# Optimization experiments

Measured on AMD Instinct MI355X. Metric: run time of the kernel, lower is better.

## Reference

```python
import jax, jax.numpy as jnp
import numpy as np

N = 100000        # nodes (== node_num)
E = 3200000       # edges
C = 8             # hidden (sparse=False branch)
HEADS = 2
GROUPS = 8
LAYERS = 3
FEAT = 16
EMB = 8
NCLS = 2


def glin(x, W, b):
    # PyG grouped Linear: x [..., C], W [G, C//G, C//G], b [C]
    G, cin, cout = W.shape
    xg = x.reshape(*x.shape[:-1], G, cin)
    out = jnp.einsum('...gi,gio->...go', xg, W)
    return out.reshape(*x.shape[:-1], G * cout) + b


def gcn_norm(edge_index, num_nodes):
    # symmetric GCN normalization with added self-loops, unit edge weights
    loop = jnp.arange(num_nodes, dtype=edge_index.dtype)
    src = jnp.concatenate([edge_index[0], loop])
    dst = jnp.concatenate([edge_index[1], loop])
    w = jnp.ones(src.shape[0], dtype=jnp.float32)
    deg = jax.ops.segment_sum(w, dst, num_segments=num_nodes)
    dinv = jnp.where(deg > 0, jax.lax.rsqrt(deg), 0.0)
    return src, dst, dinv[src] * dinv[dst]


def dna_conv(x_all, src, dst, norm, Wq, bq, Wk, bk, Wv, bv):
    # PyG DNAConv (eval mode): target's latest history entry attends over the
    # source neighbor's full history. x_all: [N, L, C].
    n, L, c = x_all.shape
    d = c // HEADS
    # q/k/v linears are per-entry -> compute per node, gather per edge (same math)
    q = glin(x_all[:, -1], Wq, bq).reshape(n, HEADS, d)    # [N,H,d]
    k = glin(x_all, Wk, bk).reshape(n, L, HEADS, d)        # [N,L,H,d]
    v = glin(x_all, Wv, bv).reshape(n, L, HEADS, d)
    qe = q[dst]                                            # [E',H,d]
    score = jnp.einsum('ehd,elhd->ehl', qe, k[src]) * (1.0 / np.sqrt(d))
    attn = jax.nn.softmax(score, axis=-1)                  # softmax over history L
    out = jnp.einsum('ehl,elhd->ehd', attn, v[src]).reshape(-1, c)
    out = out * norm[:, None]
    return jax.ops.segment_sum(out, dst, num_segments=n)   # aggr='add' at target


def setup_inputs():
    ks = jax.random.split(jax.random.key(0), 16)
    s = 0.5
    return {
        'x': jax.random.normal(ks[0], (N, FEAT), dtype=jnp.float32),
        'node_index': jnp.arange(N),
        'node_one_hot': jnp.zeros((N,), dtype=jnp.int32),
        'edge_index': jax.random.randint(ks[1], (2, E), 0, N),
        'edge_weight': jax.random.uniform(ks[2], (E,), dtype=jnp.float32),
        'emb_table': jax.random.normal(ks[3], (N, EMB), dtype=jnp.float32) * 0.1,
        'W1': jax.random.normal(ks[4], (EMB + FEAT, C), dtype=jnp.float32) * 0.2,
        'b1': jnp.zeros((C,), dtype=jnp.float32),
        'Wq': jax.random.normal(ks[5], (LAYERS, GROUPS, C // GROUPS, C // GROUPS), dtype=jnp.float32) * s,
        'bq': jnp.zeros((LAYERS, C), dtype=jnp.float32),
        'Wk': jax.random.normal(ks[6], (LAYERS, GROUPS, C // GROUPS, C // GROUPS), dtype=jnp.float32) * s,
        'bk': jnp.zeros((LAYERS, C), dtype=jnp.float32),
        'Wv': jax.random.normal(ks[7], (LAYERS, GROUPS, C // GROUPS, C // GROUPS), dtype=jnp.float32) * s,
        'bv': jnp.zeros((LAYERS, C), dtype=jnp.float32),
        'W2': jax.random.normal(ks[8], (C, NCLS), dtype=jnp.float32) * 0.3,
        'b2': jnp.zeros((NCLS,), dtype=jnp.float32),
    }


def reference(x, node_index, node_one_hot, edge_index, edge_weight,
              emb_table, W1, b1, Wq, bq, Wk, bk, Wv, bv, W2, b2):
    # node_one_hot / edge_weight are unpacked but unused in the original forward
    h = jnp.concatenate([emb_table[node_index], x], axis=1)   # [N, EMB+FEAT]
    h = jax.nn.relu(h @ W1 + b1)                              # [N, C]
    x_all = h[:, None, :]                                     # history [N, 1, C]
    src, dst, norm = gcn_norm(edge_index, x.shape[0])
    for i in range(LAYERS):
        h = jax.nn.relu(dna_conv(x_all, src, dst, norm,
                                 Wq[i], bq[i], Wk[i], bk[i], Wv[i], bv[i]))
        x_all = jnp.concatenate([x_all, h[:, None, :]], axis=1)
    logits = x_all[:, -1] @ W2 + b2
    return jax.nn.log_softmax(logits, axis=-1)
```

## Files before the change

### kernel.cpp

```cpp
#include <hip/hip_runtime.h>
#include <math.h>


#define SBB   8
#define SBN   256
#define CH    4096
#define CAP   9216

typedef _Float16 half8 __attribute__((ext_vector_type(8)));
typedef int int4v __attribute__((ext_vector_type(4)));

__global__ void __launch_bounds__(256) phaseAC(const int* __restrict__ eidx,
                                               int* __restrict__ gcnt,
                                               int* __restrict__ ebuf,
                                               int E, int NS) {
    __shared__ int sorted_[CH];
    __shared__ unsigned short karr[CH];
    __shared__ int cntS[512];
    __shared__ int lofs[512];
    __shared__ int wbase[512];
    __shared__ int sA[512], sB[512];
    int t = threadIdx.x, b = blockIdx.x;
    int base = b * CH;
    int nEdge = E - base; if (nEdge > CH) nEdge = CH;

    for (int i = t; i < 512; i += 256) cntS[i] = 0;
    __syncthreads();

    int w[16]; short kk[16];
#pragma unroll
    for (int it = 0; it < 4; it++) {
        int e0 = base + (it * 256 + t) * 4;
        if (e0 + 3 < E) {
            int4v s4 = __builtin_nontemporal_load((const int4v*)(eidx + e0));
            int4v d4 = __builtin_nontemporal_load((const int4v*)(eidx + E + e0));
#pragma unroll
            for (int j = 0; j < 4; j++) {
                int idx = it * 4 + j;
                w[idx] = s4[j] | ((d4[j] & (SBN - 1)) << 17);
                kk[idx] = (short)(d4[j] >> SBB);
                atomicAdd(&cntS[kk[idx]], 1);
            }
        } else {
#pragma unroll
            for (int j = 0; j < 4; j++) {
                int e = e0 + j, idx = it * 4 + j;
                if (e < E) {
                    int s = eidx[e], d = eidx[E + e];
                    w[idx] = s | ((d & (SBN - 1)) << 17);
                    kk[idx] = (short)(d >> SBB);
                    atomicAdd(&cntS[kk[idx]], 1);
                } else { w[idx] = 0; kk[idx] = 511; }
            }
        }
    }
    __syncthreads();
    sA[t] = cntS[t]; sA[t + 256] = cntS[t + 256];
    __syncthreads();
    int* sp = sA; int* dp = sB;
    for (int o = 1; o < 512; o <<= 1) {
#pragma unroll
        for (int h = 0; h < 2; h++) {
            int i = t + h * 256;
            int v = sp[i];
            if (i >= o) v += sp[i - o];
            dp[i] = v;
        }
        __syncthreads();
        int* tmp = sp; sp = dp; dp = tmp;
    }
    for (int i = t; i < 512; i += 256) {
        int excl = sp[i] - cntS[i];
        lofs[i] = excl;
        if (i < NS && cntS[i] > 0) {
            int g = atomicAdd(&gcnt[i], cntS[i]);
            wbase[i] = i * CAP + g - excl;
        }
    }
    __syncthreads();
#pragma unroll
    for (int idx = 0; idx < 16; idx++) {
        if (kk[idx] != 511) {
            int p = atomicAdd(&lofs[kk[idx]], 1);
            sorted_[p] = w[idx];
            karr[p] = (unsigned short)kk[idx];
        }
    }
    __syncthreads();
    for (int i = t; i < nEdge; i += 256)
        ebuf[wbase[karr[i]] + i] = sorted_[i];
}

__global__ void super_csr(int* __restrict__ ebuf, const int* __restrict__ gcnt,
                          unsigned int* __restrict__ off, char* __restrict__ A,
                          char* __restrict__ U, int NS, int n) {
    __shared__ int seg[CAP];
    __shared__ int cnt[SBN];
    __shared__ int fillp[SBN];
    __shared__ int sd[256];
    int t = threadIdx.x, k = blockIdx.x;
    cnt[t] = 0;
    int start = k * CAP;
    int len = gcnt[k];
    __syncthreads();
    for (int i = t; i < len; i += 256) {
        int w = __builtin_nontemporal_load(&ebuf[start + i]);
        seg[i] = w;
        atomicAdd(&cnt[w >> 17], 1);
    }
    __syncthreads();
    int v = cnt[t];
    sd[t] = v; __syncthreads();
    for (int o = 1; o < 256; o <<= 1) {
        int u = 0; if (t >= o) u = sd[t - o];
        __syncthreads(); sd[t] += u; __syncthreads();
    }
    int excl = sd[t] - v;
    fillp[t] = excl;
    int d = (k << SBB) + t;
    if (d < n) {
        off[d] = (unsigned int)(start + excl) | ((unsigned int)v << 22);
        float dvv = rsqrtf((float)(v + 1));
        *(float*)(A + (size_t)d * 32 + 16) = dvv;
        *(float*)(U + (size_t)d * 64 + 48) = dvv;
    }
    __syncthreads();
    for (int i = t; i < len; i += 256) {
        int w = seg[i];
        int pos = atomicAdd(&fillp[w >> 17], 1);
        ebuf[start + pos] = w & 131071;
    }
}

__global__ void node_init(const float* __restrict__ x, const int* __restrict__ nidx,
                          const float* __restrict__ emb, const float* __restrict__ W1,
                          const float* __restrict__ b1, char* __restrict__ A,
                          char* __restrict__ U, int* __restrict__ gcnt,
                          int NS, int n) {
    int i = blockIdx.x * blockDim.x + threadIdx.x;
    if (i < NS) gcnt[i] = 0;
    if (i >= n) return;
    float in[24];
    int ni = nidx[i];
    const float4* ep = (const float4*)(emb + (size_t)ni * 8);
    float4 e0 = ep[0], e1 = ep[1];
    in[0] = e0.x; in[1] = e0.y; in[2] = e0.z; in[3] = e0.w;
    in[4] = e1.x; in[5] = e1.y; in[6] = e1.z; in[7] = e1.w;
    const float4* xp = (const float4*)(x + (size_t)i * 16);
#pragma unroll
    for (int t = 0; t < 4; t++) {
        float4 v = xp[t];
        in[8 + 4 * t + 0] = v.x; in[8 + 4 * t + 1] = v.y;
        in[8 + 4 * t + 2] = v.z; in[8 + 4 * t + 3] = v.w;
    }
    float acc[8];
#pragma unroll
    for (int j = 0; j < 8; j++) acc[j] = b1[j];
#pragma unroll
    for (int t = 0; t < 24; t++) {
        float xv = in[t];
#pragma unroll
        for (int j = 0; j < 8; j++) acc[j] = fmaf(xv, W1[t * 8 + j], acc[j]);
    }
    half8 h;
#pragma unroll
    for (int j = 0; j < 8; j++) h[j] = (_Float16)fmaxf(acc[j], 0.0f);
    *(half8*)(A + (size_t)i * 32) = h;
    *(half8*)(U + (size_t)i * 64) = h;
}

template <int Li, bool LAST>
__global__ void __launch_bounds__(256, 2)
agg_layer(const int* __restrict__ ssrc, const unsigned int* __restrict__ off,
          const char* __restrict__ A, char* __restrict__ U,
          const float* __restrict__ wq, const float* __restrict__ bq,
          const float* __restrict__ wk, const float* __restrict__ bk,
          const float* __restrict__ wv, const float* __restrict__ bv,
          const float* __restrict__ W2, const float* __restrict__ b2,
          float* __restrict__ out, int n) {
    constexpr int B = 8;
    int tid = blockIdx.x * blockDim.x + threadIdx.x;
    int d = tid >> 3, t = tid & 7;
    if (d >= n) return;
    unsigned int ow = off[d];
    int lo = (int)(ow & 0x3FFFFFu), cnt = (int)(ow >> 22);

    float qk[8];
    if (Li >= 2) {
        half8 qh = (Li == 2) ? *(const half8*)(U + (size_t)d * 64 + 16)
                             : *(const half8*)(U + (size_t)d * 64 + 32);
#pragma unroll
        for (int c = 0; c < 8; c++) {
            float qv = fmaf((float)qh[c], wq[c], bq[c]);
            qk[c] = 0.5f * wk[c] * qv;
        }
    }

    float T[8]; float SN = 0.f;
#pragma unroll
    for (int c = 0; c < 8; c++) T[c] = 0.f;

    int total = cnt + 1;
    int g = (total + 7) >> 3;
    int j0 = t * g;
    int j1 = j0 + g; if (j1 > total) j1 = total;

    for (int j = j0; j < j1; j += B) {
        int m = j1 - j; if (m > B) m = B;
        int sidx[B];
#pragma unroll
        for (int u = 0; u < B; u++) {
            int idx = j + u;
            sidx[u] = (u < m) ? ((idx == 0) ? d : ssrc[lo + idx - 1]) : d;
        }
        half8 r[B][Li]; float nsv[B];
#pragma unroll
        for (int u = 0; u < B; u++) {
            if (u < m) {
                if (Li == 1) {
                    const char* p = A + (size_t)sidx[u] * 32;
                    r[u][0] = *(const half8*)p;
                    nsv[u] = *(const float*)(p + 16);
                } else {
                    const char* p = U + (size_t)sidx[u] * 64;
#pragma unroll
                    for (int l = 0; l < Li; l++) r[u][l] = *(const half8*)(p + l * 16);
                    nsv[u] = *(const float*)(p + 48);
                }
            }
        }
#pragma unroll
        for (int u = 0; u < B; u++) {
            if (u < m) {
                float xs[8 * Li];
#pragma unroll
                for (int l = 0; l < Li; l++)
#pragma unroll
                    for (int c = 0; c < 8; c++) xs[l * 8 + c] = (float)r[u][l][c];
                float ns = nsv[u];
                if (Li == 1) {
#pragma unroll
                    for (int c = 0; c < 8; c++) T[c] = fmaf(ns, xs[c], T[c]);
                    SN += ns;
                } else {
                    float score[2][Li];
#pragma unroll
                    for (int l = 0; l < Li; l++) {
#pragma unroll
                        for (int h = 0; h < 2; h++) {
                            float sc = 0.f;
#pragma unroll
                            for (int dd = 0; dd < 4; dd++) {
                                int c = h * 4 + dd;
                                sc = fmaf(qk[c], xs[l * 8 + c], sc);
                            }
                            score[h][l] = sc;
                        }
                    }
                    float e[2][Li], nsh[2];
#pragma unroll
                    for (int h = 0; h < 2; h++) {
                        float mx = score[h][0];
#pragma unroll
                        for (int l = 1; l < Li; l++) mx = fmaxf(mx, score[h][l]);
                        float ssum = 0.f;
#pragma unroll
                        for (int l = 0; l < Li; l++) { e[h][l] = __expf(score[h][l] - mx); ssum += e[h][l]; }
                        nsh[h] = ns / ssum;
                    }
#pragma unroll
                    for (int c = 0; c < 8; c++) {
                        int h = c >> 2;
                        float P = 0.f;
#pragma unroll
                        for (int l = 0; l < Li; l++) P = fmaf(e[h][l], xs[l * 8 + c], P);
                        T[c] = fmaf(nsh[h], P, T[c]);
                    }
                    SN += ns;
                }
            }
        }
    }
#pragma unroll
    for (int m2 = 1; m2 < 8; m2 <<= 1) {
#pragma unroll
        for (int c = 0; c < 8; c++) T[c] += __shfl_xor(T[c], m2);
        SN += __shfl_xor(SN, m2);
    }
    float nd = (Li == 1) ? *(const float*)(A + (size_t)d * 32 + 16)
                         : *(const float*)(U + (size_t)d * 64 + 48);
    if (!LAST) {
        float acc = fmaf(wv[t], T[t], bv[t] * SN);
        float h = fmaxf(acc * nd, 0.f);
        *(_Float16*)(U + (size_t)d * 64 + Li * 16 + 2 * t) = (_Float16)h;
    } else if (t == 0) {
        float z0 = b2[0], z1 = b2[1];
#pragma unroll
        for (int c = 0; c < 8; c++) {
            float acc = fmaf(wv[c], T[c], bv[c] * SN);
            float h = fmaxf(acc * nd, 0.f);
            z0 = fmaf(h, W2[c * 2 + 0], z0);
            z1 = fmaf(h, W2[c * 2 + 1], z1);
        }
        float m2 = fmaxf(z0, z1);
        float lse = m2 + logf(__expf(z0 - m2) + __expf(z1 - m2));
        ((float2*)out)[d] = make_float2(z0 - lse, z1 - lse);
    }
}

extern "C" void kernel_launch(void* const* d_in, const int* in_sizes, int n_in,
                              void* d_out, int out_size, void* d_ws, size_t ws_size,
                              hipStream_t stream) {
    const float* x    = (const float*)d_in[0];
    const int*   nidx = (const int*)d_in[1];
    const int*   eidx = (const int*)d_in[3];
    const float* emb  = (const float*)d_in[5];
    const float* W1   = (const float*)d_in[6];
    const float* b1   = (const float*)d_in[7];
    const float* Wq   = (const float*)d_in[8];
    const float* bq   = (const float*)d_in[9];
    const float* Wk   = (const float*)d_in[10];
    const float* bk   = (const float*)d_in[11];
    const float* Wv   = (const float*)d_in[12];
    const float* bv   = (const float*)d_in[13];
    const float* W2   = (const float*)d_in[14];
    const float* b2   = (const float*)d_in[15];
    float* out = (float*)d_out;

    const int n = in_sizes[0] / 16;
    const int E = in_sizes[3] / 2;
    const int NS = (n + SBN - 1) / SBN;
    const int NBLK = (E + CH - 1) / CH;

    char* wsp = (char*)d_ws;
    char*  A     = wsp;                      wsp += (size_t)n * 32;
    char*  U     = wsp;                      wsp += (size_t)n * 64;
    int*   ebuf  = (int*)wsp;                wsp += (size_t)NS * CAP * 4;
    unsigned int* off = (unsigned int*)wsp;  wsp += (size_t)n * 4;
    int*   gcnt  = (int*)wsp;                wsp += (size_t)NS * 4;

    dim3 blk(256);
    dim3 gn((n + 255) / 256);
    dim3 ga(((size_t)n * 8 + 255) / 256);

    node_init<<<gn, blk, 0, stream>>>(x, nidx, emb, W1, b1, A, U, gcnt, NS, n);
    phaseAC<<<NBLK, blk, 0, stream>>>(eidx, gcnt, ebuf, E, NS);
    super_csr<<<NS, blk, 0, stream>>>(ebuf, gcnt, off, A, U, NS, n);

    agg_layer<1, false><<<ga, blk, 0, stream>>>(ebuf, off, A, U,
        Wq, bq, Wk, bk, Wv, bv, W2, b2, out, n);
    agg_layer<2, false><<<ga, blk, 0, stream>>>(ebuf, off, A, U,
        Wq + 8, bq + 8, Wk + 8, bk + 8, Wv + 8, bv + 8, W2, b2, out, n);
    agg_layer<3, true><<<ga, blk, 0, stream>>>(ebuf, off, A, U,
        Wq + 16, bq + 16, Wk + 16, bk + 16, Wv + 16, bv + 16, W2, b2, out, n);
}
```

Baseline: 269.0 us.

## Pack quantized source norm into edge index and interleave edge traversal

Layer one writes each source's normalization factor, quantized to 15 bits, into the upper bits of the sorted source-index array. Later layers then read the norm from that same word instead of gathering a separate float from the node row. Edge iteration changes from contiguous per-thread chunks to a stride-8 interleave so that lanes read neighbouring edges together, and edge-index loads become nontemporal. The softmax now uses exp2 with a pre-scaled log2e constant and a hardware reciprocal. The batch size for later layers is reduced and occupancy is raised to three blocks. Risks: quantizing the norm loses precision, the packing assumes node ids fit in 17 bits, and the kernel now writes to an input buffer.

```diff
diff --git a/kernel.cpp b/kernel.cpp
--- a/kernel.cpp
+++ b/kernel.cpp
@@ -170,21 +170,24 @@
 }
 
 template <int Li, bool LAST>
-__global__ void __launch_bounds__(256, 2)
-agg_layer(const int* __restrict__ ssrc, const unsigned int* __restrict__ off,
+__global__ void __launch_bounds__(256, 3)
+agg_layer(int* __restrict__ ssrc, const unsigned int* __restrict__ off,
           const char* __restrict__ A, char* __restrict__ U,
           const float* __restrict__ wq, const float* __restrict__ bq,
           const float* __restrict__ wk, const float* __restrict__ bk,
           const float* __restrict__ wv, const float* __restrict__ bv,
           const float* __restrict__ W2, const float* __restrict__ b2,
           float* __restrict__ out, int n) {
-    constexpr int B = 8;
+    constexpr int B = (Li == 1) ? 8 : 4;
     int tid = blockIdx.x * blockDim.x + threadIdx.x;
     int d = tid >> 3, t = tid & 7;
     if (d >= n) return;
     unsigned int ow = off[d];
     int lo = (int)(ow & 0x3FFFFFu), cnt = (int)(ow >> 22);
 
+    float nd = (Li == 1) ? *(const float*)(A + (size_t)d * 32 + 16)
+                         : *(const float*)(U + (size_t)d * 64 + 48);
+
     float qk[8];
     if (Li >= 2) {
         half8 qh = (Li == 2) ? *(const half8*)(U + (size_t)d * 64 + 16)
@@ -192,7 +195,7 @@
 #pragma unroll
         for (int c = 0; c < 8; c++) {
             float qv = fmaf((float)qh[c], wq[c], bq[c]);
-            qk[c] = 0.5f * wk[c] * qv;
+            qk[c] = 0.72134752f * wk[c] * qv;
         }
     }
 
@@ -201,31 +204,32 @@
     for (int c = 0; c < 8; c++) T[c] = 0.f;
 
     int total = cnt + 1;
-    int g = (total + 7) >> 3;
-    int j0 = t * g;
-    int j1 = j0 + g; if (j1 > total) j1 = total;
-
-    for (int j = j0; j < j1; j += B) {
-        int m = j1 - j; if (m > B) m = B;
-        int sidx[B];
+
+    for (int s0 = t; s0 < total; s0 += 8 * B) {
+        int m = (total - s0 + 7) >> 3; if (m > B) m = B;
+        unsigned int w[B]; int si[B]; float ns[B];
+        half8 r[B][Li];
 #pragma unroll
         for (int u = 0; u < B; u++) {
-            int idx = j + u;
-            sidx[u] = (u < m) ? ((idx == 0) ? d : ssrc[lo + idx - 1]) : d;
-        }
-        half8 r[B][Li]; float nsv[B];
+            int s = s0 + 8 * u;
+            w[u] = 0u;
+            if (u < m && s > 0)
+                w[u] = (unsigned int)__builtin_nontemporal_load(ssrc + lo + s - 1);
+        }
 #pragma unroll
         for (int u = 0; u < B; u++) {
             if (u < m) {
+                int s = s0 + 8 * u;
+                si[u] = (s == 0) ? d : (int)(w[u] & 0x1FFFFu);
                 if (Li == 1) {
-                    const char* p = A + (size_t)sidx[u] * 32;
+                    const char* p = A + (size_t)si[u] * 32;
                     r[u][0] = *(const half8*)p;
-                    nsv[u] = *(const float*)(p + 16);
+                    ns[u] = (s == 0) ? nd : *(const float*)(p + 16);
                 } else {
-                    const char* p = U + (size_t)sidx[u] * 64;
+                    const char* p = U + (size_t)si[u] * 64;
 #pragma unroll
                     for (int l = 0; l < Li; l++) r[u][l] = *(const half8*)(p + l * 16);
-                    nsv[u] = *(const float*)(p + 48);
+                    ns[u] = (s == 0) ? nd : (float)(w[u] >> 17) * (1.0f / 32767.0f);
                 }
             }
         }
@@ -237,11 +241,11 @@
                 for (int l = 0; l < Li; l++)
 #pragma unroll
                     for (int c = 0; c < 8; c++) xs[l * 8 + c] = (float)r[u][l][c];
-                float ns = nsv[u];
+                float nv = ns[u];
                 if (Li == 1) {
 #pragma unroll
-                    for (int c = 0; c < 8; c++) T[c] = fmaf(ns, xs[c], T[c]);
-                    SN += ns;
+                    for (int c = 0; c < 8; c++) T[c] = fmaf(nv, xs[c], T[c]);
+                    SN += nv;
                 } else {
                     float score[2][Li];
 #pragma unroll
@@ -265,8 +269,8 @@
                         for (int l = 1; l < Li; l++) mx = fmaxf(mx, score[h][l]);
                         float ssum = 0.f;
 #pragma unroll
-                        for (int l = 0; l < Li; l++) { e[h][l] = __expf(score[h][l] - mx); ssum += e[h][l]; }
-                        nsh[h] = ns / ssum;
+                        for (int l = 0; l < Li; l++) { e[h][l] = exp2f(score[h][l] - mx); ssum += e[h][l]; }
+                        nsh[h] = nv * __builtin_amdgcn_rcpf(ssum);
                     }
 #pragma unroll
                     for (int c = 0; c < 8; c++) {
@@ -276,7 +280,18 @@
                         for (int l = 0; l < Li; l++) P = fmaf(e[h][l], xs[l * 8 + c], P);
                         T[c] = fmaf(nsh[h], P, T[c]);
                     }
-                    SN += ns;
+                    SN += nv;
+                }
+            }
+        }
+        if (Li == 1) {
+#pragma unroll
+            for (int u = 0; u < B; u++) {
+                int s = s0 + 8 * u;
+                if (u < m && s > 0) {
+                    unsigned int q = (unsigned int)(ns[u] * 32767.0f + 0.5f);
+                    int packed = (int)(w[u] | (q << 17));
+                    __builtin_nontemporal_store(packed, ssrc + lo + s - 1);
                 }
             }
         }
@@ -287,8 +302,6 @@
         for (int c = 0; c < 8; c++) T[c] += __shfl_xor(T[c], m2);
         SN += __shfl_xor(SN, m2);
     }
-    float nd = (Li == 1) ? *(const float*)(A + (size_t)d * 32 + 16)
-                         : *(const float*)(U + (size_t)d * 64 + 48);
     if (!LAST) {
         float acc = fmaf(wv[t], T[t], bv[t] * SN);
         float h = fmaxf(acc * nd, 0.f);
```

Result: slower. 276.9 us (+2.9%).
